# Kernel tuning notes

Hardware: AMD Instinct MI355X
Metric: run time of the kernel (lower is better)

Reference implementation:

```python
import jax, jax.numpy as jnp
import numpy as np

B = 96   # batch (must equal C for the residual broadcast to be legal)
C = 96   # num_channels == seq_len (x is (B, C, 1, C))
S = 96   # sequence length = C
NH = 8   # num_heads
DK = 96  # d_k (defaults to num_channels)
G = 8    # groupnorm groups
EPS = 1e-5


def setup_inputs() -> dict:
    key = jax.random.key(0)
    ks = jax.random.split(key, 9)
    D = NH * DK
    scale = 0.05
    return {
        "x": jax.random.normal(ks[0], (B, C, 1, C), jnp.float32),
        "Wq": jax.random.normal(ks[1], (C, D), jnp.float32) * scale,
        "bq": jax.random.normal(ks[2], (D,), jnp.float32) * scale,
        "Wk": jax.random.normal(ks[3], (C, D), jnp.float32) * scale,
        "bk": jax.random.normal(ks[4], (D,), jnp.float32) * scale,
        "Wv": jax.random.normal(ks[5], (C, D), jnp.float32) * scale,
        "bv": jax.random.normal(ks[6], (D,), jnp.float32) * scale,
        "Wo": jax.random.normal(ks[7], (D, C), jnp.float32) * scale,
        "bo": jax.random.normal(ks[8], (C,), jnp.float32) * scale,
        "gamma": jnp.ones((C,), jnp.float32),
        "beta": jnp.zeros((C,), jnp.float32),
    }


def group_norm(x, gamma, beta):
    # x: (B, C, H, W); normalize over (C//G, H, W) within each of G groups
    b, c, h, w = x.shape
    xg = x.reshape(b, G, -1)
    mu = jnp.mean(xg, axis=-1, keepdims=True)
    var = jnp.var(xg, axis=-1, keepdims=True)
    xn = ((xg - mu) * jax.lax.rsqrt(var + EPS)).reshape(b, c, h, w)
    return xn * gamma[None, :, None, None] + beta[None, :, None, None]


def reference(x, Wq, bq, Wk, bk, Wv, bv, Wo, bo, gamma, beta):
    xn = group_norm(x, gamma, beta)           # (B, C, 1, C)
    residual = xn
    t = xn.reshape(B, S, C)                   # H == 1, squeeze
    # self-attention: q = k = v = normalized x
    q = (t @ Wq + bq).reshape(B, S, NH, DK).transpose(0, 2, 1, 3)  # (B, H, S, Dk)
    k = (t @ Wk + bk).reshape(B, S, NH, DK).transpose(0, 2, 1, 3)
    v = (t @ Wv + bv).reshape(B, S, NH, DK).transpose(0, 2, 1, 3)
    scores = jnp.einsum('bhqd,bhkd->bhqk', q, k) / jnp.sqrt(jnp.float32(DK))
    causal = jnp.tril(jnp.ones((S, S), bool))  # mask=True -> causal tril mask
    scores = jnp.where(causal[None, None], scores, -jnp.inf)
    attn = jax.nn.softmax(scores, axis=-1)
    out = jnp.einsum('bhqk,bhkd->bhqd', attn, v)       # (B, H, S, Dk)
    out = out.transpose(0, 2, 1, 3).reshape(B, S, NH * DK)
    out = out @ Wo + bo                                # (B, S, C); dropout(p=0) = id
    # faithful to the source: (B,S,C) + (B,C,1,C) broadcasts to (B,C,S,C)
    return out + residual
```

## Files before the change

### kernel.cpp

```cpp
#include <hip/hip_runtime.h>
#include <hip/hip_bf16.h>

#define BATCH 96
#define CH    96
#define SEQ   96
#define NHEAD 8
#define DK    96
#define DMODEL 768
#define GRP   8
#define EPSV  1e-5f

typedef __bf16 bf16x8 __attribute__((ext_vector_type(8)));
typedef float  f32x4  __attribute__((ext_vector_type(4)));
typedef unsigned short u16;

#define MFMA16(a, b, c) __builtin_amdgcn_mfma_f32_16x16x32_bf16((a), (b), (c), 0, 0, 0)

__device__ __forceinline__ u16 f2bf(float f) {
    union { float f; unsigned int u; } c; c.f = f;
    unsigned int u = c.u + 0x7fffu + ((c.u >> 16) & 1u);
    return (u16)(u >> 16);
}

__global__ __launch_bounds__(128) void prep_kernel(
        const float* __restrict__ x, const float* __restrict__ gamma,
        const float* __restrict__ beta,
        const float* __restrict__ Wq, const float* __restrict__ Wk,
        const float* __restrict__ Wv, const float* __restrict__ Wo,
        float* __restrict__ xn, u16* __restrict__ xn_bf,
        u16* __restrict__ WqT, u16* __restrict__ WkT,
        u16* __restrict__ WvT, u16* __restrict__ WoT) {
    if (blockIdx.x < 768) {
        int bg = blockIdx.x;
        int b = bg >> 3, g = bg & 7;
        const float* xp = x + b * 9216 + g * 1152;
        float vals[9];
        float s = 0.f, ss = 0.f;
        #pragma unroll
        for (int r = 0; r < 9; ++r) {
            float v = xp[threadIdx.x + 128 * r];
            vals[r] = v; s += v; ss += v * v;
        }
        #pragma unroll
        for (int off = 32; off > 0; off >>= 1) {
            s  += __shfl_down(s, off);
            ss += __shfl_down(ss, off);
        }
        __shared__ float red[4];
        if ((threadIdx.x & 63) == 0) {
            red[(threadIdx.x >> 6) * 2]     = s;
            red[(threadIdx.x >> 6) * 2 + 1] = ss;
        }
        __syncthreads();
        s = red[0] + red[2]; ss = red[1] + red[3];
        float mu   = s * (1.0f / 1152.0f);
        float var  = ss * (1.0f / 1152.0f) - mu * mu;
        float rsig = rsqrtf(var + EPSV);
        #pragma unroll
        for (int r = 0; r < 9; ++r) {
            int e = threadIdx.x + 128 * r;
            int c = g * 12 + e / 96;
            float v = (vals[r] - mu) * rsig * gamma[c] + beta[c];
            int idx = b * 9216 + g * 1152 + e;
            xn[idx]    = v;
            xn_bf[idx] = f2bf(v);
        }
    } else {
        int t = blockIdx.x - 768;
        int seg = t / 576;
        int idx = (t - seg * 576) * 128 + threadIdx.x;
        const float* src = seg == 0 ? Wq : seg == 1 ? Wk : seg == 2 ? Wv : Wo;
        u16* dst = seg == 0 ? WqT : seg == 1 ? WkT : seg == 2 ? WvT : WoT;
        float v = src[idx];
        if (seg < 3) {
            int k2 = idx / 768, n = idx - k2 * 768;
            dst[n * 96 + k2] = f2bf(v);
        } else {
            int k2 = idx / 96, n = idx - k2 * 96;
            dst[n * 768 + k2] = f2bf(v);
        }
    }
}

__global__ __launch_bounds__(384) void fattn_kernel(
        const u16* __restrict__ xn_bf,
        const u16* __restrict__ WqT, const u16* __restrict__ WkT,
        const u16* __restrict__ WvT,
        const float* __restrict__ bq, const float* __restrict__ bk,
        const float* __restrict__ bv,
        u16* __restrict__ attn_out) {
    int b = blockIdx.x >> 3, h = blockIdx.x & 7;
    __shared__ __align__(16) u16 qb[96][104];
    __shared__ __align__(16) u16 kb[96][104];
    __shared__ __align__(16) u16 vt[96][104];

    int wave = threadIdx.x >> 6, lane = threadIdx.x & 63;
    int ln = lane & 15, quad = lane >> 4;
    int m0 = wave * 16;
    const u16* xb = xn_bf + b * 9216;
    const int hq = h * 96;

    bf16x8 a[3], av[3];
    #pragma unroll
    for (int kt = 0; kt < 3; ++kt) {
        a[kt]  = *(const bf16x8*)(xb + (m0 + ln) * 96 + kt * 32 + quad * 8);
        av[kt] = *(const bf16x8*)(WvT + (hq + m0 + ln) * 96 + kt * 32 + quad * 8);
    }

    float bvr[4];
    #pragma unroll
    for (int r = 0; r < 4; ++r) bvr[r] = bv[hq + m0 + quad * 4 + r];
    f32x4 aq[6], ak[6], avv[6];
    #pragma unroll
    for (int nt = 0; nt < 6; ++nt) {
        float bqc = bq[hq + nt * 16 + ln];
        float bkc = bk[hq + nt * 16 + ln];
        aq[nt]  = f32x4{bqc, bqc, bqc, bqc};
        ak[nt]  = f32x4{bkc, bkc, bkc, bkc};
        avv[nt] = f32x4{bvr[0], bvr[1], bvr[2], bvr[3]};
    }

    #pragma unroll
    for (int kt = 0; kt < 3; ++kt)
        #pragma unroll
        for (int nt = 0; nt < 6; ++nt) {
            bf16x8 bqf = *(const bf16x8*)(WqT + (hq + nt * 16 + ln) * 96 + kt * 32 + quad * 8);
            aq[nt] = MFMA16(a[kt], bqf, aq[nt]);
        }
    #pragma unroll
    for (int kt = 0; kt < 3; ++kt)
        #pragma unroll
        for (int nt = 0; nt < 6; ++nt) {
            bf16x8 bkf = *(const bf16x8*)(WkT + (hq + nt * 16 + ln) * 96 + kt * 32 + quad * 8);
            ak[nt] = MFMA16(a[kt], bkf, ak[nt]);
        }
    #pragma unroll
    for (int kt = 0; kt < 3; ++kt)
        #pragma unroll
        for (int nt = 0; nt < 6; ++nt) {
            bf16x8 bvf = *(const bf16x8*)(xb + (nt * 16 + ln) * 96 + kt * 32 + quad * 8);
            avv[nt] = MFMA16(av[kt], bvf, avv[nt]);
        }

    #pragma unroll
    for (int nt = 0; nt < 6; ++nt) {
        int col = nt * 16 + ln;
        #pragma unroll
        for (int r = 0; r < 4; ++r) {
            int row = m0 + quad * 4 + r;
            qb[row][col] = f2bf(aq[nt][r]);
            kb[row][col] = f2bf(ak[nt][r]);
            vt[row][col] = f2bf(avv[nt][r]);
        }
    }
    __syncthreads();

    f32x4 accs[6] = {};
    #pragma unroll
    for (int kt = 0; kt < 3; ++kt) {
        bf16x8 aa = *(const bf16x8*)(&qb[m0 + ln][kt * 32 + quad * 8]);
        #pragma unroll
        for (int nt = 0; nt < 6; ++nt) {
            bf16x8 bb = *(const bf16x8*)(&kb[nt * 16 + ln][kt * 32 + quad * 8]);
            accs[nt] = MFMA16(aa, bb, accs[nt]);
        }
    }

    const float scale = 0.10206207261596577f;
    float pout[4][6];
    #pragma unroll
    for (int r = 0; r < 4; ++r) {
        int row = m0 + quad * 4 + r;
        float vals[6], m = -1e30f;
        #pragma unroll
        for (int nt = 0; nt < 6; ++nt) {
            int col = nt * 16 + ln;
            float sv = accs[nt][r] * scale;
            vals[nt] = (col <= row) ? sv : -1e30f;
            m = fmaxf(m, vals[nt]);
        }
        #pragma unroll
        for (int off = 1; off < 16; off <<= 1) m = fmaxf(m, __shfl_xor(m, off));
        float sum = 0.f;
        #pragma unroll
        for (int nt = 0; nt < 6; ++nt) {
            float p = (vals[nt] > -1e29f) ? __expf(vals[nt] - m) : 0.f;
            pout[r][nt] = p; sum += p;
        }
        #pragma unroll
        for (int off = 1; off < 16; off <<= 1) sum += __shfl_xor(sum, off);
        float rinv = 1.0f / sum;
        #pragma unroll
        for (int nt = 0; nt < 6; ++nt) pout[r][nt] *= rinv;
    }
    __syncthreads();
    #pragma unroll
    for (int r = 0; r < 4; ++r)
        #pragma unroll
        for (int nt = 0; nt < 6; ++nt)
            kb[m0 + quad * 4 + r][nt * 16 + ln] = f2bf(pout[r][nt]);
    __syncthreads();

    f32x4 acco[6] = {};
    #pragma unroll
    for (int kt = 0; kt < 3; ++kt) {
        bf16x8 aa = *(const bf16x8*)(&kb[m0 + ln][kt * 32 + quad * 8]);
        #pragma unroll
        for (int nt = 0; nt < 6; ++nt) {
            bf16x8 bb = *(const bf16x8*)(&vt[nt * 16 + ln][kt * 32 + quad * 8]);
            acco[nt] = MFMA16(aa, bb, acco[nt]);
        }
    }
    const size_t obase = (size_t)b * 96 * DMODEL + hq;
    #pragma unroll
    for (int nt = 0; nt < 6; ++nt) {
        int d = nt * 16 + ln;
        #pragma unroll
        for (int r = 0; r < 4; ++r) {
            int row = m0 + quad * 4 + r;
            attn_out[obase + (size_t)row * DMODEL + d] = f2bf(acco[nt][r]);
        }
    }
}

__global__ __launch_bounds__(384) void obcast_kernel(
        const u16* __restrict__ attn, const u16* __restrict__ WoT,
        const float* __restrict__ bo, const float* __restrict__ xn,
        float* __restrict__ out) {
    __shared__ __align__(16) float red[6][16][96];
    __shared__ __align__(16) float xnt[24][96];
    int wave = threadIdx.x >> 6, lane = threadIdx.x & 63;
    int ln = lane & 15, quad = lane >> 4;

    int bid = blockIdx.x;
    int iq = bid & 3;
    int jk = bid >> 2;
    int j  = jk / 6;
    int k0 = (jk - j * 6) * 16;
    int m0 = jk * 16;
    int i0 = iq * 24;

    {
        const f32x4* xn4 = (const f32x4*)xn;
        f32x4* xt4 = (f32x4*)xnt;
        int idx = threadIdx.x;
        int i = idx / 24, l4 = idx - i * 24;
        xt4[idx] = xn4[(size_t)((i0 + i) * 96 + j) * 24 + l4];
        if (threadIdx.x < 192) {
            int idx2 = threadIdx.x + 384;
            int i2 = idx2 / 24, l42 = idx2 - i2 * 24;
            xt4[idx2] = xn4[(size_t)((i0 + i2) * 96 + j) * 24 + l42];
        }
    }

    int kw = wave * 128;
    f32x4 acc[6] = {};
    #pragma unroll
    for (int kt = 0; kt < 4; ++kt) {
        bf16x8 a = *(const bf16x8*)(attn + (size_t)(m0 + ln) * DMODEL + kw + kt * 32 + quad * 8);
        #pragma unroll
        for (int nt = 0; nt < 6; ++nt) {
            bf16x8 bb = *(const bf16x8*)(WoT + (nt * 16 + ln) * DMODEL + kw + kt * 32 + quad * 8);
            acc[nt] = MFMA16(a, bb, acc[nt]);
        }
    }
    #pragma unroll
    for (int nt = 0; nt < 6; ++nt)
        #pragma unroll
        for (int r = 0; r < 4; ++r)
            red[wave][quad * 4 + r][nt * 16 + ln] = acc[nt][r];
    __syncthreads();

    #pragma unroll
    for (int e = 0; e < 4; ++e) {
        int idx = threadIdx.x + e * 384;
        int row = idx / 96, col = idx - row * 96;
        red[0][row][col] = red[0][row][col] + red[1][row][col] +
                           red[2][row][col] + red[3][row][col] +
                           red[4][row][col] + red[5][row][col] + bo[col];
    }
    __syncthreads();

    f32x4* out4 = (f32x4*)out;
    const f32x4* pt4 = (const f32x4*)red;
    const f32x4* xt4 = (const f32x4*)xnt;
    int k  = threadIdx.x / 24;
    int l4 = threadIdx.x - k * 24;
    f32x4 pv = pt4[k * 24 + l4];
    size_t o = ((size_t)(i0 * 96 + j) * 96 + (k0 + k)) * 24 + l4;
    #pragma unroll
    for (int i = 0; i < 24; ++i) {
        f32x4 rr = pv + xt4[i * 24 + l4];
        __builtin_nontemporal_store(rr, &out4[o]);
        o += 221184;
    }
}

extern "C" void kernel_launch(void* const* d_in, const int* in_sizes, int n_in,
                              void* d_out, int out_size, void* d_ws, size_t ws_size,
                              hipStream_t stream) {
    const float* x     = (const float*)d_in[0];
    const float* Wq    = (const float*)d_in[1];
    const float* bq    = (const float*)d_in[2];
    const float* Wk    = (const float*)d_in[3];
    const float* bk    = (const float*)d_in[4];
    const float* Wv    = (const float*)d_in[5];
    const float* bv    = (const float*)d_in[6];
    const float* Wo    = (const float*)d_in[7];
    const float* bo    = (const float*)d_in[8];
    const float* gamma = (const float*)d_in[9];
    const float* beta  = (const float*)d_in[10];
    float* out = (float*)d_out;

    char* ws = (char*)d_ws;
    float* xn_f = (float*)(ws + 0);
    u16*  xn_b  = (u16*)(ws + 3538944);
    u16*  WqT   = (u16*)(ws + 5308416);
    u16*  WkT   = (u16*)(ws + 5455872);
    u16*  WvT   = (u16*)(ws + 5603328);
    u16*  WoT   = (u16*)(ws + 5750784);
    u16*  ab    = (u16*)(ws + 5898240);

    prep_kernel<<<dim3(3072), dim3(128), 0, stream>>>(
        x, gamma, beta, Wq, Wk, Wv, Wo, xn_f, xn_b, WqT, WkT, WvT, WoT);
    fattn_kernel<<<dim3(BATCH * NHEAD), dim3(384), 0, stream>>>(
        xn_b, WqT, WkT, WvT, bq, bk, bv, ab);
    obcast_kernel<<<dim3(2304), dim3(384), 0, stream>>>(ab, WoT, bo, xn_f, out);
}
```

Baseline: 407.8 us.

## Split fused attention into separate QKV projection and per-wave attention kernels

Replaces the single fused per-(batch,head) attention kernel with two kernels. The first computes Q, K and V^T projections on a 3D grid (one projection per block) and writes them to global memory. The second computes attention with independent waves, each owning 16 query rows and using only a small private LDS tile, so no block-wide barriers are needed. This raises parallelism and removes syncthreads, at the cost of an extra launch and roughly 42MB of extra global traffic for the Q/K/V round trip.

```diff
diff --git a/kernel.cpp b/kernel.cpp
--- a/kernel.cpp
+++ b/kernel.cpp
@@ -82,89 +82,91 @@
     }
 }
 
-__global__ __launch_bounds__(384) void fattn_kernel(
+__global__ __launch_bounds__(384) void qkv_kernel(
         const u16* __restrict__ xn_bf,
         const u16* __restrict__ WqT, const u16* __restrict__ WkT,
         const u16* __restrict__ WvT,
         const float* __restrict__ bq, const float* __restrict__ bk,
         const float* __restrict__ bv,
-        u16* __restrict__ attn_out) {
-    int b = blockIdx.x >> 3, h = blockIdx.x & 7;
-    __shared__ __align__(16) u16 qb[96][104];
-    __shared__ __align__(16) u16 kb[96][104];
-    __shared__ __align__(16) u16 vt[96][104];
-
+        u16* __restrict__ qs, u16* __restrict__ ks, u16* __restrict__ vts) {
+    int bh = blockIdx.x, seg = blockIdx.y;
+    int b = bh >> 3, h = bh & 7;
     int wave = threadIdx.x >> 6, lane = threadIdx.x & 63;
     int ln = lane & 15, quad = lane >> 4;
-    int m0 = wave * 16;
+    int m0 = wave * 16, hq = h * 96;
     const u16* xb = xn_bf + b * 9216;
-    const int hq = h * 96;
-
-    bf16x8 a[3], av[3];
-    #pragma unroll
-    for (int kt = 0; kt < 3; ++kt) {
-        a[kt]  = *(const bf16x8*)(xb + (m0 + ln) * 96 + kt * 32 + quad * 8);
-        av[kt] = *(const bf16x8*)(WvT + (hq + m0 + ln) * 96 + kt * 32 + quad * 8);
-    }
-
-    float bvr[4];
-    #pragma unroll
-    for (int r = 0; r < 4; ++r) bvr[r] = bv[hq + m0 + quad * 4 + r];
-    f32x4 aq[6], ak[6], avv[6];
-    #pragma unroll
-    for (int nt = 0; nt < 6; ++nt) {
-        float bqc = bq[hq + nt * 16 + ln];
-        float bkc = bk[hq + nt * 16 + ln];
-        aq[nt]  = f32x4{bqc, bqc, bqc, bqc};
-        ak[nt]  = f32x4{bkc, bkc, bkc, bkc};
-        avv[nt] = f32x4{bvr[0], bvr[1], bvr[2], bvr[3]};
-    }
-
+
+    const u16* abase;
+    const u16* bbase;
+    u16* dst;
+    if (seg == 0)      { abase = xb + (m0 + ln) * 96;        bbase = WqT + hq * 96; dst = qs; }
+    else if (seg == 1) { abase = xb + (m0 + ln) * 96;        bbase = WkT + hq * 96; dst = ks; }
+    else               { abase = WvT + (hq + m0 + ln) * 96;  bbase = xb;            dst = vts; }
+
+    bf16x8 a[3];
     #pragma unroll
     for (int kt = 0; kt < 3; ++kt)
-        #pragma unroll
-        for (int nt = 0; nt < 6; ++nt) {
-            bf16x8 bqf = *(const bf16x8*)(WqT + (hq + nt * 16 + ln) * 96 + kt * 32 + quad * 8);
-            aq[nt] = MFMA16(a[kt], bqf, aq[nt]);
-        }
+        a[kt] = *(const bf16x8*)(abase + kt * 32 + quad * 8);
+
+    f32x4 acc[6];
+    if (seg == 2) {
+        float b0 = bv[hq + m0 + quad * 4];
+        float b1 = bv[hq + m0 + quad * 4 + 1];
+        float b2 = bv[hq + m0 + quad * 4 + 2];
+        float b3 = bv[hq + m0 + quad * 4 + 3];
+        #pragma unroll
+        for (int nt = 0; nt < 6; ++nt) acc[nt] = f32x4{b0, b1, b2, b3};
+    } else {
+        const float* bias = (seg == 0) ? bq : bk;
+        #pragma unroll
+        for (int nt = 0; nt < 6; ++nt) {
+            float c = bias[hq + nt * 16 + ln];
+            acc[nt] = f32x4{c, c, c, c};
+        }
+    }
+
     #pragma unroll
     for (int kt = 0; kt < 3; ++kt)
         #pragma unroll
         for (int nt = 0; nt < 6; ++nt) {
-            bf16x8 bkf = *(const bf16x8*)(WkT + (hq + nt * 16 + ln) * 96 + kt * 32 + quad * 8);
-            ak[nt] = MFMA16(a[kt], bkf, ak[nt]);
-        }
+            bf16x8 bb = *(const bf16x8*)(bbase + (nt * 16 + ln) * 96 + kt * 32 + quad * 8);
+            acc[nt] = MFMA16(a[kt], bb, acc[nt]);
+        }
+
+    u16* o = dst + (size_t)bh * 9216;
+    #pragma unroll
+    for (int nt = 0; nt < 6; ++nt)
+        #pragma unroll
+        for (int r = 0; r < 4; ++r)
+            o[(m0 + quad * 4 + r) * 96 + nt * 16 + ln] = f2bf(acc[nt][r]);
+}
+
+__global__ __launch_bounds__(256) void attn_kernel(
+        const u16* __restrict__ qs, const u16* __restrict__ ks,
+        const u16* __restrict__ vts, u16* __restrict__ ab) {
+    __shared__ __align__(16) u16 pb[4][16][104];
+    int wave = threadIdx.x >> 6, lane = threadIdx.x & 63;
+    int ln = lane & 15, quad = lane >> 4;
+    unsigned w = blockIdx.x * 4 + wave;
+    unsigned bh = w / 6;
+    int m0 = (int)(w - bh * 6) * 16;
+    int b = bh >> 3, h = bh & 7;
+    const u16* q  = qs  + (size_t)bh * 9216;
+    const u16* k  = ks  + (size_t)bh * 9216;
+    const u16* vt = vts + (size_t)bh * 9216;
+
+    bf16x8 aa[3];
     #pragma unroll
     for (int kt = 0; kt < 3; ++kt)
-        #pragma unroll
-        for (int nt = 0; nt < 6; ++nt) {
-            bf16x8 bvf = *(const bf16x8*)(xb + (nt * 16 + ln) * 96 + kt * 32 + quad * 8);
-            avv[nt] = MFMA16(av[kt], bvf, avv[nt]);
-        }
-
-    #pragma unroll
-    for (int nt = 0; nt < 6; ++nt) {
-        int col = nt * 16 + ln;
-        #pragma unroll
-        for (int r = 0; r < 4; ++r) {
-            int row = m0 + quad * 4 + r;
-            qb[row][col] = f2bf(aq[nt][r]);
-            kb[row][col] = f2bf(ak[nt][r]);
-            vt[row][col] = f2bf(avv[nt][r]);
-        }
-    }
-    __syncthreads();
-
+        aa[kt] = *(const bf16x8*)(q + (m0 + ln) * 96 + kt * 32 + quad * 8);
     f32x4 accs[6] = {};
     #pragma unroll
-    for (int kt = 0; kt < 3; ++kt) {
-        bf16x8 aa = *(const bf16x8*)(&qb[m0 + ln][kt * 32 + quad * 8]);
-        #pragma unroll
-        for (int nt = 0; nt < 6; ++nt) {
-            bf16x8 bb = *(const bf16x8*)(&kb[nt * 16 + ln][kt * 32 + quad * 8]);
-            accs[nt] = MFMA16(aa, bb, accs[nt]);
-        }
-    }
+    for (int kt = 0; kt < 3; ++kt)
+        #pragma unroll
+        for (int nt = 0; nt < 6; ++nt) {
+            bf16x8 bb = *(const bf16x8*)(k + (nt * 16 + ln) * 96 + kt * 32 + quad * 8);
+            accs[nt] = MFMA16(aa[kt], bb, accs[nt]);
+        }
 
     const float scale = 0.10206207261596577f;
     float pout[4][6];
@@ -193,32 +195,31 @@
         #pragma unroll
         for (int nt = 0; nt < 6; ++nt) pout[r][nt] *= rinv;
     }
-    __syncthreads();
+
     #pragma unroll
     for (int r = 0; r < 4; ++r)
         #pragma unroll
         for (int nt = 0; nt < 6; ++nt)
-            kb[m0 + quad * 4 + r][nt * 16 + ln] = f2bf(pout[r][nt]);
-    __syncthreads();
+            pb[wave][quad * 4 + r][nt * 16 + ln] = f2bf(pout[r][nt]);
 
     f32x4 acco[6] = {};
     #pragma unroll
     for (int kt = 0; kt < 3; ++kt) {
-        bf16x8 aa = *(const bf16x8*)(&kb[m0 + ln][kt * 32 + quad * 8]);
-        #pragma unroll
-        for (int nt = 0; nt < 6; ++nt) {
-            bf16x8 bb = *(const bf16x8*)(&vt[nt * 16 + ln][kt * 32 + quad * 8]);
-            acco[nt] = MFMA16(aa, bb, acco[nt]);
-        }
-    }
-    const size_t obase = (size_t)b * 96 * DMODEL + hq;
+        bf16x8 pa = *(const bf16x8*)(&pb[wave][ln][kt * 32 + quad * 8]);
+        #pragma unroll
+        for (int nt = 0; nt < 6; ++nt) {
+            bf16x8 bb = *(const bf16x8*)(vt + (nt * 16 + ln) * 96 + kt * 32 + quad * 8);
+            acco[nt] = MFMA16(pa, bb, acco[nt]);
+        }
+    }
+    const size_t obase = (size_t)b * 96 * DMODEL + h * 96;
     #pragma unroll
     for (int nt = 0; nt < 6; ++nt) {
         int d = nt * 16 + ln;
         #pragma unroll
         for (int r = 0; r < 4; ++r) {
             int row = m0 + quad * 4 + r;
-            attn_out[obase + (size_t)row * DMODEL + d] = f2bf(acco[nt][r]);
+            ab[obase + (size_t)row * DMODEL + d] = f2bf(acco[nt][r]);
         }
     }
 }
@@ -319,11 +320,15 @@
     u16*  WkT   = (u16*)(ws + 5455872);
     u16*  WvT   = (u16*)(ws + 5603328);
     u16*  WoT   = (u16*)(ws + 5750784);
-    u16*  ab    = (u16*)(ws + 5898240);
+    u16*  qsb   = (u16*)(ws + 5898240);
+    u16*  ksb   = (u16*)(ws + 20054016);
+    u16*  vtsb  = (u16*)(ws + 34209792);
+    u16*  ab    = (u16*)(ws + 48365568);
 
     prep_kernel<<<dim3(3072), dim3(128), 0, stream>>>(
         x, gamma, beta, Wq, Wk, Wv, Wo, xn_f, xn_b, WqT, WkT, WvT, WoT);
-    fattn_kernel<<<dim3(BATCH * NHEAD), dim3(384), 0, stream>>>(
-        xn_b, WqT, WkT, WvT, bq, bk, bv, ab);
+    qkv_kernel<<<dim3(768, 3), dim3(384), 0, stream>>>(
+        xn_b, WqT, WkT, WvT, bq, bk, bv, qsb, ksb, vtsb);
+    attn_kernel<<<dim3(1152), dim3(256), 0, stream>>>(qsb, ksb, vtsb, ab);
     obcast_kernel<<<dim3(2304), dim3(384), 0, stream>>>(ab, WoT, bo, xn_f, out);
 }
```

Result: slower. 421.4 us (+3.3%).
